# Optimization experiments

Hardware: AMD Instinct MI355X
Metric: run time of the kernel (lower is better)

The kernel has to match this reference:

```python
import jax, jax.numpy as jnp
import numpy as np

EPS = 1e-15  # matches torch_geometric GMMConv


def setup_inputs() -> dict:
    key = jax.random.key(0)
    ks = jax.random.split(key, 8)
    N, E, C_in, C_out, K, D = 163842, 1146894, 32, 32, 6, 3
    x = jax.random.normal(ks[0], (N, C_in), dtype=jnp.float32)
    edge_index = jax.random.randint(ks[1], (2, E), 0, N, dtype=jnp.int64)
    pseudo = jax.random.uniform(ks[2], (E, D), dtype=jnp.float32)
    g = jax.random.normal(ks[3], (C_in, K * C_out), dtype=jnp.float32) / np.sqrt(C_in)
    mu = jax.random.normal(ks[4], (K, D), dtype=jnp.float32)
    sigma = jax.random.uniform(ks[5], (K, D), dtype=jnp.float32) + 0.5
    root = jax.random.normal(ks[6], (C_in, C_out), dtype=jnp.float32) / np.sqrt(C_in)
    bias = jnp.zeros((C_out,), dtype=jnp.float32)
    return {"x": x, "edge_index": edge_index, "pseudo": pseudo, "g": g,
            "mu": mu, "sigma": sigma, "root": root, "bias": bias}


def reference(x, edge_index, pseudo, g, mu, sigma, root, bias):
    N = x.shape[0]
    K, D = mu.shape
    C_out = g.shape[1] // K
    src, dst = edge_index[0], edge_index[1]
    # per-node transform then gather per edge: [N, K, C_out] -> [E, K, C_out]
    xg = (x @ g).reshape(N, K, C_out)
    # Gaussian mixture weights on edge pseudo-coordinates: [E, K]
    diff = pseudo[:, None, :] - mu[None, :, :]              # [E, K, D]
    gauss = jnp.exp(jnp.sum(-0.5 * diff * diff / (EPS + sigma * sigma)[None], axis=-1))
    # weighted sum over kernels -> per-edge message [E, C_out]
    msg = jnp.einsum('eko,ek->eo', xg[src], gauss)
    # mean aggregation at destination nodes
    agg = jax.ops.segment_sum(msg, dst, num_segments=N)
    cnt = jax.ops.segment_sum(jnp.ones((src.shape[0],), x.dtype), dst, num_segments=N)
    out = agg / jnp.maximum(cnt, 1.0)[:, None]
    # root weight and bias (PyG defaults root_weight=True, bias=True)
    return out + x @ root + bias
```

## Files before the change

kernel.cpp:

```cpp
#include <hip/hip_runtime.h>
#include <hip/hip_bf16.h>

#define KD 6
#define DD 3
#define CO 32
#define CI 32
#define KC (KD * CO)
#define QP (KC / 2)
#define SCAN_T 256
#define SCAN_B 2048

__device__ __forceinline__ uint pack_bf16(float a, float b) {
    uint lo = (uint)__bfloat16_as_ushort(__float2bfloat16(a));
    uint hi = (uint)__bfloat16_as_ushort(__float2bfloat16(b));
    return lo | (hi << 16);
}
__device__ __forceinline__ float bf_lo(uint u) { return __uint_as_float(u << 16); }
__device__ __forceinline__ float bf_hi(uint u) { return __uint_as_float(u & 0xffff0000u); }

__global__ __launch_bounds__(256, 4)
void xg_kernel(const float* __restrict__ x, const float* __restrict__ g,
               uint* __restrict__ xg, int N) {
    __shared__ float gs[CI * KC];
    for (int i = threadIdx.x; i < CI * KC; i += blockDim.x) gs[i] = g[i];
    __syncthreads();
    const int NP = (N + 1) >> 1;
    const int total = NP * 48;
    for (int idx = blockIdx.x * blockDim.x + threadIdx.x; idx < total;
         idx += gridDim.x * blockDim.x) {
        const int rp = idx / 48;
        const int t = idx - rp * 48;
        const int n0 = rp * 2;
        const int n1 = (n0 + 1 < N) ? (n0 + 1) : n0;
        const float* xr0 = x + (size_t)n0 * CI;
        const float* xr1 = x + (size_t)n1 * CI;
        float a00 = 0.f, a01 = 0.f, a02 = 0.f, a03 = 0.f;
        float a10 = 0.f, a11 = 0.f, a12 = 0.f, a13 = 0.f;
#pragma unroll 2
        for (int c = 0; c < CI; c += 4) {
            const float4 xv0 = *(const float4*)&xr0[c];
            const float4 xv1 = *(const float4*)&xr1[c];
            const float4 g0 = *(const float4*)&gs[(c + 0) * KC + 4 * t];
            const float4 g1 = *(const float4*)&gs[(c + 1) * KC + 4 * t];
            const float4 g2 = *(const float4*)&gs[(c + 2) * KC + 4 * t];
            const float4 g3 = *(const float4*)&gs[(c + 3) * KC + 4 * t];
            a00 = fmaf(xv0.x, g0.x, a00); a01 = fmaf(xv0.x, g0.y, a01);
            a02 = fmaf(xv0.x, g0.z, a02); a03 = fmaf(xv0.x, g0.w, a03);
            a10 = fmaf(xv1.x, g0.x, a10); a11 = fmaf(xv1.x, g0.y, a11);
            a12 = fmaf(xv1.x, g0.z, a12); a13 = fmaf(xv1.x, g0.w, a13);
            a00 = fmaf(xv0.y, g1.x, a00); a01 = fmaf(xv0.y, g1.y, a01);
            a02 = fmaf(xv0.y, g1.z, a02); a03 = fmaf(xv0.y, g1.w, a03);
            a10 = fmaf(xv1.y, g1.x, a10); a11 = fmaf(xv1.y, g1.y, a11);
            a12 = fmaf(xv1.y, g1.z, a12); a13 = fmaf(xv1.y, g1.w, a13);
            a00 = fmaf(xv0.z, g2.x, a00); a01 = fmaf(xv0.z, g2.y, a01);
            a02 = fmaf(xv0.z, g2.z, a02); a03 = fmaf(xv0.z, g2.w, a03);
            a10 = fmaf(xv1.z, g2.x, a10); a11 = fmaf(xv1.z, g2.y, a11);
            a12 = fmaf(xv1.z, g2.z, a12); a13 = fmaf(xv1.z, g2.w, a13);
            a00 = fmaf(xv0.w, g3.x, a00); a01 = fmaf(xv0.w, g3.y, a01);
            a02 = fmaf(xv0.w, g3.z, a02); a03 = fmaf(xv0.w, g3.w, a03);
            a10 = fmaf(xv1.w, g3.x, a10); a11 = fmaf(xv1.w, g3.y, a11);
            a12 = fmaf(xv1.w, g3.z, a12); a13 = fmaf(xv1.w, g3.w, a13);
        }
        uint2 pk0 = make_uint2(pack_bf16(a00, a01), pack_bf16(a02, a03));
        *(uint2*)(xg + (size_t)n0 * QP + 2 * t) = pk0;
        if (n0 + 1 < N) {
            uint2 pk1 = make_uint2(pack_bf16(a10, a11), pack_bf16(a12, a13));
            *(uint2*)(xg + (size_t)(n0 + 1) * QP + 2 * t) = pk1;
        }
    }
}

__global__ void hist_kernel(const int* __restrict__ ei, int* __restrict__ hist, int E) {
    for (int e = blockIdx.x * blockDim.x + threadIdx.x; e < E;
         e += gridDim.x * blockDim.x)
        atomicAdd(&hist[ei[E + e]], 1);
}

__global__ void scanA_kernel(const int* __restrict__ hist, int* __restrict__ incl,
                             int* __restrict__ sums, int N) {
    __shared__ int lds[SCAN_T];
    const int t = threadIdx.x;
    const int base = blockIdx.x * SCAN_B + t * 8;
    int v[8]; int ts = 0;
#pragma unroll
    for (int j = 0; j < 8; ++j) { v[j] = (base + j < N) ? hist[base + j] : 0; ts += v[j]; }
    lds[t] = ts; __syncthreads();
    int acc = ts;
    for (int off = 1; off < SCAN_T; off <<= 1) {
        int add = (t >= off) ? lds[t - off] : 0;
        __syncthreads();
        acc += add; lds[t] = acc;
        __syncthreads();
    }
    int run = acc - ts;
#pragma unroll
    for (int j = 0; j < 8; ++j) { run += v[j]; if (base + j < N) incl[base + j] = run; }
    if (t == SCAN_T - 1) sums[blockIdx.x] = acc;
}

__global__ void scanB_kernel(int* __restrict__ sums, int nb) {
    __shared__ int lds[SCAN_T];
    const int t = threadIdx.x;
    int v = (t < nb) ? sums[t] : 0;
    lds[t] = v; __syncthreads();
    int acc = v;
    for (int off = 1; off < SCAN_T; off <<= 1) {
        int add = (t >= off) ? lds[t - off] : 0;
        __syncthreads();
        acc += add; lds[t] = acc;
        __syncthreads();
    }
    if (t < nb) sums[t] = acc - v;
}

__global__ void scanC_kernel(const int* __restrict__ incl, const int* __restrict__ sums,
                             const int* __restrict__ hist, int* __restrict__ row_start,
                             int* __restrict__ cursor, int N) {
    const int i = blockIdx.x * blockDim.x + threadIdx.x;
    if (i == 0) row_start[0] = 0;
    if (i < N) {
        const int fin = incl[i] + sums[i / SCAN_B];
        row_start[i + 1] = fin;
        cursor[i] = fin - hist[i];
    }
}

__global__ void scatter_kernel(const int* __restrict__ ei, const float* __restrict__ pseudo,
                               const float* __restrict__ mu, const float* __restrict__ sigma,
                               int* __restrict__ cursor, uint4* __restrict__ sorted, int E) {
    float m[KD][DD], iv[KD][DD];
#pragma unroll
    for (int k = 0; k < KD; ++k)
#pragma unroll
        for (int d = 0; d < DD; ++d) {
            m[k][d] = mu[k * DD + d];
            float s = sigma[k * DD + d];
            iv[k][d] = -0.5f / (1e-15f + s * s);
        }
    for (int e = blockIdx.x * blockDim.x + threadIdx.x; e < E;
         e += gridDim.x * blockDim.x) {
        const int src = ei[e];
        const int dst = ei[E + e];
        const float p0 = pseudo[3 * e], p1 = pseudo[3 * e + 1], p2 = pseudo[3 * e + 2];
        float w[KD];
#pragma unroll
        for (int k = 0; k < KD; ++k) {
            float d0 = p0 - m[k][0], d1 = p1 - m[k][1], d2 = p2 - m[k][2];
            w[k] = __expf(d0 * d0 * iv[k][0] + d1 * d1 * iv[k][1] + d2 * d2 * iv[k][2]);
        }
        const int pos = atomicAdd(&cursor[dst], 1);
        sorted[pos] = make_uint4((uint)src, pack_bf16(w[0], w[1]),
                                 pack_bf16(w[2], w[3]), pack_bf16(w[4], w[5]));
    }
}

__global__ void agg_kernel(const uint4* __restrict__ sorted, const uint* __restrict__ xg,
                           const int* __restrict__ row_start, float* __restrict__ out, int N) {
    const int l = threadIdx.x & 31;
    const int kbase = l >> 4;
    const int p = l & 15;
    const int d = (blockIdx.x * blockDim.x + threadIdx.x) >> 5;
    if (d >= N) return;
    const int s = row_start[d];
    const int t = row_start[d + 1];
    float s0 = 0.f, s1 = 0.f;
    for (int i = s; i < t; ++i) {
        const uint4 rec = sorted[i];
        const float wa = __uint_as_float((kbase ? (rec.y >> 16) : (rec.y & 0xffffu)) << 16);
        const float wb = __uint_as_float((kbase ? (rec.z >> 16) : (rec.z & 0xffffu)) << 16);
        const float wc = __uint_as_float((kbase ? (rec.w >> 16) : (rec.w & 0xffffu)) << 16);
        const uint* xr = xg + (size_t)rec.x * QP;
        const uint u0 = xr[l];
        const uint u1 = xr[l + 32];
        const uint u2 = xr[l + 64];
        s0 = fmaf(wa, bf_lo(u0), s0); s1 = fmaf(wa, bf_hi(u0), s1);
        s0 = fmaf(wb, bf_lo(u1), s0); s1 = fmaf(wb, bf_hi(u1), s1);
        s0 = fmaf(wc, bf_lo(u2), s0); s1 = fmaf(wc, bf_hi(u2), s1);
    }
    s0 += __shfl_xor(s0, 16);
    s1 += __shfl_xor(s1, 16);
    const float inv = 1.0f / fmaxf((float)(t - s), 1.0f);
    out[(size_t)d * CO + 2 * p + kbase] = (kbase ? s1 : s0) * inv;
}

__global__ void out_kernel(const float* __restrict__ x, const float* __restrict__ root,
                           const float* __restrict__ bias, float* __restrict__ out, int N) {
    __shared__ float rs[CI * CO];
    __shared__ float bs[CO];
    for (int i = threadIdx.x; i < CI * CO; i += blockDim.x) rs[i] = root[i];
    if (threadIdx.x < CO) bs[threadIdx.x] = bias[threadIdx.x];
    __syncthreads();
    const int total = N * 8;
    for (int idx = blockIdx.x * blockDim.x + threadIdx.x; idx < total;
         idx += gridDim.x * blockDim.x) {
        const int n = idx >> 3;
        const int t = idx & 7;
        const float* xr = x + (size_t)n * CI;
        float a0 = 0.f, a1 = 0.f, a2 = 0.f, a3 = 0.f;
#pragma unroll
        for (int c = 0; c < CI; ++c) {
            const float4 rv = *(const float4*)&rs[c * CO + 4 * t];
            float xc = xr[c];
            a0 = fmaf(xc, rv.x, a0);
            a1 = fmaf(xc, rv.y, a1);
            a2 = fmaf(xc, rv.z, a2);
            a3 = fmaf(xc, rv.w, a3);
        }
        float4 o = *(float4*)&out[(size_t)n * CO + 4 * t];
        const float4 bv = *(const float4*)&bs[4 * t];
        o.x = o.x + a0 + bv.x;
        o.y = o.y + a1 + bv.y;
        o.z = o.z + a2 + bv.z;
        o.w = o.w + a3 + bv.w;
        *(float4*)&out[(size_t)n * CO + 4 * t] = o;
    }
}

extern "C" void kernel_launch(void* const* d_in, const int* in_sizes, int n_in,
                              void* d_out, int out_size, void* d_ws, size_t ws_size,
                              hipStream_t stream) {
    const float* x      = (const float*)d_in[0];
    const int*   ei     = (const int*)d_in[1];
    const float* pseudo = (const float*)d_in[2];
    const float* g      = (const float*)d_in[3];
    const float* mu     = (const float*)d_in[4];
    const float* sigma  = (const float*)d_in[5];
    const float* root   = (const float*)d_in[6];
    const float* bias   = (const float*)d_in[7];
    float* out = (float*)d_out;

    const int N = in_sizes[0] / CI;
    const int E = in_sizes[1] / 2;

    uint* xg       = (uint*)d_ws;
    int*  hist     = (int*)(xg + (size_t)N * QP);
    int*  incl     = hist + N;
    int*  row_start= incl + N;
    int*  cursor   = row_start + N + 1;
    int*  sums     = cursor + N;
    uint4* sorted  = (uint4*)(((uintptr_t)(sums + SCAN_T) + 15) & ~(uintptr_t)15);

    hipMemsetAsync(hist, 0, (size_t)N * sizeof(int), stream);

    const int blk = 256;

    xg_kernel<<<2048, blk, 0, stream>>>(x, g, xg, N);

    hist_kernel<<<2048, blk, 0, stream>>>(ei, hist, E);

    const int nb = (N + SCAN_B - 1) / SCAN_B;
    scanA_kernel<<<nb, SCAN_T, 0, stream>>>(hist, incl, sums, N);
    scanB_kernel<<<1, SCAN_T, 0, stream>>>(sums, nb);
    scanC_kernel<<<(N + blk - 1) / blk, blk, 0, stream>>>(incl, sums, hist, row_start,
                                                         cursor, N);

    scatter_kernel<<<2048, blk, 0, stream>>>(ei, pseudo, mu, sigma, cursor, sorted, E);

    agg_kernel<<<(N * 32 + blk - 1) / blk, blk, 0, stream>>>(sorted, xg, row_start, out, N);

    int grid3 = (N * 8 + blk - 1) / blk;
    if (grid3 > 4096) grid3 = 4096;
    out_kernel<<<grid3, blk, 0, stream>>>(x, root, bias, out, N);
}
```

Baseline: 375.6 us.

## Fuse root transform into aggregation, widen xg rows, unroll edge loop

The root-weight matmul and bias are folded into the aggregation kernel's epilogue, so the separate output kernel and its read-modify-write of the output disappear. The xg kernel now computes four node rows per thread instead of two, reusing each shared-memory g load across more rows. The scatter kernel switches from a grid-stride loop to one edge per thread with a full grid, and the aggregation loop processes two edges per iteration to overlap gathers. Costs are more register pressure in xg, a root-matrix load into shared memory in every aggregation block, and a per-thread 32-element dot product there.

```diff
diff --git a/kernel.cpp b/kernel.cpp
--- a/kernel.cpp
+++ b/kernel.cpp
@@ -17,6 +17,9 @@
 }
 __device__ __forceinline__ float bf_lo(uint u) { return __uint_as_float(u << 16); }
 __device__ __forceinline__ float bf_hi(uint u) { return __uint_as_float(u & 0xffff0000u); }
+__device__ __forceinline__ float selw(uint v, int kbase) {
+    return __uint_as_float((kbase ? (v >> 16) : (v & 0xffffu)) << 16);
+}
 
 __global__ __launch_bounds__(256, 4)
 void xg_kernel(const float* __restrict__ x, const float* __restrict__ g,
@@ -24,48 +27,50 @@
     __shared__ float gs[CI * KC];
     for (int i = threadIdx.x; i < CI * KC; i += blockDim.x) gs[i] = g[i];
     __syncthreads();
-    const int NP = (N + 1) >> 1;
-    const int total = NP * 48;
+    const int NB = (N + 3) >> 2;
+    const int total = NB * 48;
     for (int idx = blockIdx.x * blockDim.x + threadIdx.x; idx < total;
          idx += gridDim.x * blockDim.x) {
-        const int rp = idx / 48;
-        const int t = idx - rp * 48;
-        const int n0 = rp * 2;
-        const int n1 = (n0 + 1 < N) ? (n0 + 1) : n0;
-        const float* xr0 = x + (size_t)n0 * CI;
-        const float* xr1 = x + (size_t)n1 * CI;
-        float a00 = 0.f, a01 = 0.f, a02 = 0.f, a03 = 0.f;
-        float a10 = 0.f, a11 = 0.f, a12 = 0.f, a13 = 0.f;
+        const int b = idx / 48;
+        const int t = idx - b * 48;
+        const int n0 = b * 4;
+        size_t ro0 = (size_t)n0 * CI;
+        size_t ro1 = (size_t)((n0 + 1 < N) ? n0 + 1 : N - 1) * CI;
+        size_t ro2 = (size_t)((n0 + 2 < N) ? n0 + 2 : N - 1) * CI;
+        size_t ro3 = (size_t)((n0 + 3 < N) ? n0 + 3 : N - 1) * CI;
+        float acc[4][4];
+#pragma unroll
+        for (int r = 0; r < 4; ++r) { acc[r][0] = acc[r][1] = acc[r][2] = acc[r][3] = 0.f; }
 #pragma unroll 2
         for (int c = 0; c < CI; c += 4) {
-            const float4 xv0 = *(const float4*)&xr0[c];
-            const float4 xv1 = *(const float4*)&xr1[c];
             const float4 g0 = *(const float4*)&gs[(c + 0) * KC + 4 * t];
             const float4 g1 = *(const float4*)&gs[(c + 1) * KC + 4 * t];
             const float4 g2 = *(const float4*)&gs[(c + 2) * KC + 4 * t];
             const float4 g3 = *(const float4*)&gs[(c + 3) * KC + 4 * t];
-            a00 = fmaf(xv0.x, g0.x, a00); a01 = fmaf(xv0.x, g0.y, a01);
-            a02 = fmaf(xv0.x, g0.z, a02); a03 = fmaf(xv0.x, g0.w, a03);
-            a10 = fmaf(xv1.x, g0.x, a10); a11 = fmaf(xv1.x, g0.y, a11);
-            a12 = fmaf(xv1.x, g0.z, a12); a13 = fmaf(xv1.x, g0.w, a13);
-            a00 = fmaf(xv0.y, g1.x, a00); a01 = fmaf(xv0.y, g1.y, a01);
-            a02 = fmaf(xv0.y, g1.z, a02); a03 = fmaf(xv0.y, g1.w, a03);
-            a10 = fmaf(xv1.y, g1.x, a10); a11 = fmaf(xv1.y, g1.y, a11);
-            a12 = fmaf(xv1.y, g1.z, a12); a13 = fmaf(xv1.y, g1.w, a13);
-            a00 = fmaf(xv0.z, g2.x, a00); a01 = fmaf(xv0.z, g2.y, a01);
-            a02 = fmaf(xv0.z, g2.z, a02); a03 = fmaf(xv0.z, g2.w, a03);
-            a10 = fmaf(xv1.z, g2.x, a10); a11 = fmaf(xv1.z, g2.y, a11);
-            a12 = fmaf(xv1.z, g2.z, a12); a13 = fmaf(xv1.z, g2.w, a13);
-            a00 = fmaf(xv0.w, g3.x, a00); a01 = fmaf(xv0.w, g3.y, a01);
-            a02 = fmaf(xv0.w, g3.z, a02); a03 = fmaf(xv0.w, g3.w, a03);
-            a10 = fmaf(xv1.w, g3.x, a10); a11 = fmaf(xv1.w, g3.y, a11);
-            a12 = fmaf(xv1.w, g3.z, a12); a13 = fmaf(xv1.w, g3.w, a13);
+            const float4 xv0 = *(const float4*)&x[ro0 + c];
+            const float4 xv1 = *(const float4*)&x[ro1 + c];
+            const float4 xv2 = *(const float4*)&x[ro2 + c];
+            const float4 xv3 = *(const float4*)&x[ro3 + c];
+#define ROWFMA(r, xv)                                                          \
+            acc[r][0] = fmaf(xv.x, g0.x, acc[r][0]); acc[r][1] = fmaf(xv.x, g0.y, acc[r][1]); \
+            acc[r][2] = fmaf(xv.x, g0.z, acc[r][2]); acc[r][3] = fmaf(xv.x, g0.w, acc[r][3]); \
+            acc[r][0] = fmaf(xv.y, g1.x, acc[r][0]); acc[r][1] = fmaf(xv.y, g1.y, acc[r][1]); \
+            acc[r][2] = fmaf(xv.y, g1.z, acc[r][2]); acc[r][3] = fmaf(xv.y, g1.w, acc[r][3]); \
+            acc[r][0] = fmaf(xv.z, g2.x, acc[r][0]); acc[r][1] = fmaf(xv.z, g2.y, acc[r][1]); \
+            acc[r][2] = fmaf(xv.z, g2.z, acc[r][2]); acc[r][3] = fmaf(xv.z, g2.w, acc[r][3]); \
+            acc[r][0] = fmaf(xv.w, g3.x, acc[r][0]); acc[r][1] = fmaf(xv.w, g3.y, acc[r][1]); \
+            acc[r][2] = fmaf(xv.w, g3.z, acc[r][2]); acc[r][3] = fmaf(xv.w, g3.w, acc[r][3]);
+            ROWFMA(0, xv0) ROWFMA(1, xv1) ROWFMA(2, xv2) ROWFMA(3, xv3)
+#undef ROWFMA
         }
-        uint2 pk0 = make_uint2(pack_bf16(a00, a01), pack_bf16(a02, a03));
-        *(uint2*)(xg + (size_t)n0 * QP + 2 * t) = pk0;
-        if (n0 + 1 < N) {
-            uint2 pk1 = make_uint2(pack_bf16(a10, a11), pack_bf16(a12, a13));
-            *(uint2*)(xg + (size_t)(n0 + 1) * QP + 2 * t) = pk1;
+#pragma unroll
+        for (int r = 0; r < 4; ++r) {
+            const int n = n0 + r;
+            if (n < N) {
+                uint2 pk = make_uint2(pack_bf16(acc[r][0], acc[r][1]),
+                                      pack_bf16(acc[r][2], acc[r][3]));
+                *(uint2*)(xg + (size_t)n * QP + 2 * t) = pk;
+            }
         }
     }
 }
@@ -128,6 +133,8 @@
 __global__ void scatter_kernel(const int* __restrict__ ei, const float* __restrict__ pseudo,
                                const float* __restrict__ mu, const float* __restrict__ sigma,
                                int* __restrict__ cursor, uint4* __restrict__ sorted, int E) {
+    const int e = blockIdx.x * blockDim.x + threadIdx.x;
+    if (e >= E) return;
     float m[KD][DD], iv[KD][DD];
 #pragma unroll
     for (int k = 0; k < KD; ++k)
@@ -137,25 +144,29 @@
             float s = sigma[k * DD + d];
             iv[k][d] = -0.5f / (1e-15f + s * s);
         }
-    for (int e = blockIdx.x * blockDim.x + threadIdx.x; e < E;
-         e += gridDim.x * blockDim.x) {
-        const int src = ei[e];
-        const int dst = ei[E + e];
-        const float p0 = pseudo[3 * e], p1 = pseudo[3 * e + 1], p2 = pseudo[3 * e + 2];
-        float w[KD];
-#pragma unroll
-        for (int k = 0; k < KD; ++k) {
-            float d0 = p0 - m[k][0], d1 = p1 - m[k][1], d2 = p2 - m[k][2];
-            w[k] = __expf(d0 * d0 * iv[k][0] + d1 * d1 * iv[k][1] + d2 * d2 * iv[k][2]);
-        }
-        const int pos = atomicAdd(&cursor[dst], 1);
-        sorted[pos] = make_uint4((uint)src, pack_bf16(w[0], w[1]),
-                                 pack_bf16(w[2], w[3]), pack_bf16(w[4], w[5]));
-    }
+    const int src = ei[e];
+    const int dst = ei[E + e];
+    const float p0 = pseudo[3 * e], p1 = pseudo[3 * e + 1], p2 = pseudo[3 * e + 2];
+    float w[KD];
+#pragma unroll
+    for (int k = 0; k < KD; ++k) {
+        float d0 = p0 - m[k][0], d1 = p1 - m[k][1], d2 = p2 - m[k][2];
+        w[k] = __expf(d0 * d0 * iv[k][0] + d1 * d1 * iv[k][1] + d2 * d2 * iv[k][2]);
+    }
+    const int pos = atomicAdd(&cursor[dst], 1);
+    sorted[pos] = make_uint4((uint)src, pack_bf16(w[0], w[1]),
+                             pack_bf16(w[2], w[3]), pack_bf16(w[4], w[5]));
 }
 
 __global__ void agg_kernel(const uint4* __restrict__ sorted, const uint* __restrict__ xg,
-                           const int* __restrict__ row_start, float* __restrict__ out, int N) {
+                           const int* __restrict__ row_start, const float* __restrict__ x,
+                           const float* __restrict__ root, const float* __restrict__ bias,
+                           float* __restrict__ out, int N) {
+    __shared__ float rs[CI * CO];
+    __shared__ float bs[CO];
+    for (int i = threadIdx.x; i < CI * CO; i += blockDim.x) rs[i] = root[i];
+    if (threadIdx.x < CO) bs[threadIdx.x] = bias[threadIdx.x];
+    __syncthreads();
     const int l = threadIdx.x & 31;
     const int kbase = l >> 4;
     const int p = l & 15;
@@ -164,56 +175,41 @@
     const int s = row_start[d];
     const int t = row_start[d + 1];
     float s0 = 0.f, s1 = 0.f;
-    for (int i = s; i < t; ++i) {
-        const uint4 rec = sorted[i];
-        const float wa = __uint_as_float((kbase ? (rec.y >> 16) : (rec.y & 0xffffu)) << 16);
-        const float wb = __uint_as_float((kbase ? (rec.z >> 16) : (rec.z & 0xffffu)) << 16);
-        const float wc = __uint_as_float((kbase ? (rec.w >> 16) : (rec.w & 0xffffu)) << 16);
-        const uint* xr = xg + (size_t)rec.x * QP;
-        const uint u0 = xr[l];
-        const uint u1 = xr[l + 32];
-        const uint u2 = xr[l + 64];
-        s0 = fmaf(wa, bf_lo(u0), s0); s1 = fmaf(wa, bf_hi(u0), s1);
-        s0 = fmaf(wb, bf_lo(u1), s0); s1 = fmaf(wb, bf_hi(u1), s1);
-        s0 = fmaf(wc, bf_lo(u2), s0); s1 = fmaf(wc, bf_hi(u2), s1);
+    int i = s;
+    for (; i + 1 < t; i += 2) {
+        const uint4 ra = sorted[i];
+        const uint4 rb = sorted[i + 1];
+        const uint* xa = xg + (size_t)ra.x * QP;
+        const uint* xb = xg + (size_t)rb.x * QP;
+        const uint a0 = xa[l], a1 = xa[l + 32], a2 = xa[l + 64];
+        const uint b0 = xb[l], b1 = xb[l + 32], b2 = xb[l + 64];
+        float wa = selw(ra.y, kbase), wb = selw(ra.z, kbase), wc = selw(ra.w, kbase);
+        s0 = fmaf(wa, bf_lo(a0), s0); s1 = fmaf(wa, bf_hi(a0), s1);
+        s0 = fmaf(wb, bf_lo(a1), s0); s1 = fmaf(wb, bf_hi(a1), s1);
+        s0 = fmaf(wc, bf_lo(a2), s0); s1 = fmaf(wc, bf_hi(a2), s1);
+        wa = selw(rb.y, kbase); wb = selw(rb.z, kbase); wc = selw(rb.w, kbase);
+        s0 = fmaf(wa, bf_lo(b0), s0); s1 = fmaf(wa, bf_hi(b0), s1);
+        s0 = fmaf(wb, bf_lo(b1), s0); s1 = fmaf(wb, bf_hi(b1), s1);
+        s0 = fmaf(wc, bf_lo(b2), s0); s1 = fmaf(wc, bf_hi(b2), s1);
+    }
+    if (i < t) {
+        const uint4 ra = sorted[i];
+        const uint* xa = xg + (size_t)ra.x * QP;
+        const uint a0 = xa[l], a1 = xa[l + 32], a2 = xa[l + 64];
+        const float wa = selw(ra.y, kbase), wb = selw(ra.z, kbase), wc = selw(ra.w, kbase);
+        s0 = fmaf(wa, bf_lo(a0), s0); s1 = fmaf(wa, bf_hi(a0), s1);
+        s0 = fmaf(wb, bf_lo(a1), s0); s1 = fmaf(wb, bf_hi(a1), s1);
+        s0 = fmaf(wc, bf_lo(a2), s0); s1 = fmaf(wc, bf_hi(a2), s1);
     }
     s0 += __shfl_xor(s0, 16);
     s1 += __shfl_xor(s1, 16);
     const float inv = 1.0f / fmaxf((float)(t - s), 1.0f);
-    out[(size_t)d * CO + 2 * p + kbase] = (kbase ? s1 : s0) * inv;
-}
-
-__global__ void out_kernel(const float* __restrict__ x, const float* __restrict__ root,
-                           const float* __restrict__ bias, float* __restrict__ out, int N) {
-    __shared__ float rs[CI * CO];
-    __shared__ float bs[CO];
-    for (int i = threadIdx.x; i < CI * CO; i += blockDim.x) rs[i] = root[i];
-    if (threadIdx.x < CO) bs[threadIdx.x] = bias[threadIdx.x];
-    __syncthreads();
-    const int total = N * 8;
-    for (int idx = blockIdx.x * blockDim.x + threadIdx.x; idx < total;
-         idx += gridDim.x * blockDim.x) {
-        const int n = idx >> 3;
-        const int t = idx & 7;
-        const float* xr = x + (size_t)n * CI;
-        float a0 = 0.f, a1 = 0.f, a2 = 0.f, a3 = 0.f;
-#pragma unroll
-        for (int c = 0; c < CI; ++c) {
-            const float4 rv = *(const float4*)&rs[c * CO + 4 * t];
-            float xc = xr[c];
-            a0 = fmaf(xc, rv.x, a0);
-            a1 = fmaf(xc, rv.y, a1);
-            a2 = fmaf(xc, rv.z, a2);
-            a3 = fmaf(xc, rv.w, a3);
-        }
-        float4 o = *(float4*)&out[(size_t)n * CO + 4 * t];
-        const float4 bv = *(const float4*)&bs[4 * t];
-        o.x = o.x + a0 + bv.x;
-        o.y = o.y + a1 + bv.y;
-        o.z = o.z + a2 + bv.z;
-        o.w = o.w + a3 + bv.w;
-        *(float4*)&out[(size_t)n * CO + 4 * t] = o;
-    }
+    const int ch = 2 * p + kbase;
+    const float* xr = x + (size_t)d * CI;
+    float acc = 0.f;
+#pragma unroll
+    for (int c = 0; c < CI; ++c) acc = fmaf(xr[c], rs[c * CO + ch], acc);
+    out[(size_t)d * CO + ch] = (kbase ? s1 : s0) * inv + acc + bs[ch];
 }
 
 extern "C" void kernel_launch(void* const* d_in, const int* in_sizes, int n_in,
@@ -244,7 +240,8 @@
 
     const int blk = 256;
 
-    xg_kernel<<<2048, blk, 0, stream>>>(x, g, xg, N);
+    const int xg_total = ((N + 3) >> 2) * 48;
+    xg_kernel<<<(xg_total + blk - 1) / blk, blk, 0, stream>>>(x, g, xg, N);
 
     hist_kernel<<<2048, blk, 0, stream>>>(ei, hist, E);
 
@@ -254,11 +251,9 @@
     scanC_kernel<<<(N + blk - 1) / blk, blk, 0, stream>>>(incl, sums, hist, row_start,
                                                          cursor, N);
 
-    scatter_kernel<<<2048, blk, 0, stream>>>(ei, pseudo, mu, sigma, cursor, sorted, E);
-
-    agg_kernel<<<(N * 32 + blk - 1) / blk, blk, 0, stream>>>(sorted, xg, row_start, out, N);
-
-    int grid3 = (N * 8 + blk - 1) / blk;
-    if (grid3 > 4096) grid3 = 4096;
-    out_kernel<<<grid3, blk, 0, stream>>>(x, root, bias, out, N);
-}
+    scatter_kernel<<<(E + blk - 1) / blk, blk, 0, stream>>>(ei, pseudo, mu, sigma,
+                                                            cursor, sorted, E);
+
+    agg_kernel<<<(N * 32 + blk - 1) / blk, blk, 0, stream>>>(sorted, xg, row_start,
+                                                             x, root, bias, out, N);
+}
```

Result: faster. 362.9 us (-3.4%).
